# Kernel optimization log

Measured on AMD Instinct MI355X. Metric: run time of the kernel, lower is better.

Reference implementation:

```python
import jax, jax.numpy as jnp
import numpy as np

GROUPS = 8


def setup_inputs() -> dict:
    key = jax.random.key(0)
    k1, k2, k3 = jax.random.split(key, 3)
    B, H, W, Cin, Cout, KH, KW = 32, 56, 56, 256, 256, 3, 3
    inputs = jax.random.normal(k1, (B, H, W, Cin), dtype=jnp.float32)
    # HWIO kernel for grouped conv: input channel dim = Cin // groups
    fan_in = KH * KW * (Cin // GROUPS)
    limit = np.sqrt(6.0 / (fan_in + Cout // GROUPS))  # glorot-ish scale
    kernel = jax.random.uniform(k2, (KH, KW, Cin // GROUPS, Cout), dtype=jnp.float32,
                                minval=-limit, maxval=limit)
    bias = jnp.zeros((Cout,), dtype=jnp.float32)
    return {"inputs": inputs, "kernel": kernel, "bias": bias}


def reference(inputs, kernel, bias):
    # Equivalent to per-group slice + Conv2D + concat: a single grouped conv.
    # inputs: [B,H,W,Cin] NHWC; kernel: [KH,KW,Cin//G,Cout] HWIO
    out = jax.lax.conv_general_dilated(
        inputs, kernel,
        window_strides=(1, 1),
        padding="SAME",
        lhs_dilation=(1, 1),
        rhs_dilation=(1, 1),
        dimension_numbers=("NHWC", "HWIO", "NHWC"),
        feature_group_count=GROUPS,
    )
    out = out + bias  # broadcast over [B,H,W,Cout]
    return out
```

## Files before the change

kernel.cpp:

```cpp
#include <hip/hip_runtime.h>


#define R_ 8
#define TPW 7

typedef __bf16 bf16x8 __attribute__((ext_vector_type(8)));
typedef float floatx4 __attribute__((ext_vector_type(4)));
typedef unsigned short ushortx4 __attribute__((ext_vector_type(4)));

__device__ __forceinline__ unsigned short f2bf(float f) {
    unsigned int u = __builtin_bit_cast(unsigned int, f);
    u += 0x7fffu + ((u >> 16) & 1u);
    return (unsigned short)(u >> 16);
}

__global__ __launch_bounds__(256, 2)
void gconv_mfma(const float* __restrict__ in, const float* __restrict__ wgt,
                const float* __restrict__ bias, float* __restrict__ out) {
    const int rt = blockIdx.x;
    const int g  = blockIdx.y;
    const int b  = blockIdx.z;
    const int y0 = rt * R_;

    __shared__ unsigned short lds_in[10 * 58 * 32];
    __shared__ unsigned short lds_w[9 * 32 * 32];

    const int tid = threadIdx.x;

    for (int i = tid; i < 9 * 32 * 32; i += 256) {
        const int co = i & 31;
        const int ci = (i >> 5) & 31;
        const int kk = i >> 10;
        lds_w[(kk * 32 + co) * 32 + ci] = f2bf(wgt[(kk * 32 + ci) * 256 + g * 32 + co]);
    }

    for (int c = tid; c < 10 * 58 * 8; c += 256) {
        const int row = c / 464;
        const int rem = c - row * 464;
        const int col = rem >> 3;
        const int q   = rem & 7;
        const int gy = y0 - 1 + row;
        const int gx = col - 1;
        float4 v = make_float4(0.f, 0.f, 0.f, 0.f);
        if ((unsigned)gy < 56u && (unsigned)gx < 56u) {
            v = *reinterpret_cast<const float4*>(
                &in[(((b * 56 + gy) * 56 + gx) * 256) + g * 32 + q * 4]);
        }
        ushortx4 p;
        p.x = f2bf(v.x); p.y = f2bf(v.y); p.z = f2bf(v.z); p.w = f2bf(v.w);
        *reinterpret_cast<ushortx4*>(&lds_in[(row * 58 + col) * 32 + q * 4]) = p;
    }

    __syncthreads();

    const int wv   = tid >> 6;
    const int lane = tid & 63;
    const int lc   = lane & 15;
    const int quad = lane >> 4;

    int lane_base[TPW];
#pragma unroll
    for (int t = 0; t < TPW; ++t) {
        const int p  = (wv * TPW + t) * 16 + lc;
        const int yl = p / 56;
        const int xl = p - yl * 56;
        lane_base[t] = (yl * 58 + xl) * 32 + quad * 8;
    }

    floatx4 acc[TPW][2];
#pragma unroll
    for (int t = 0; t < TPW; ++t) {
        acc[t][0] = (floatx4)(0.f);
        acc[t][1] = (floatx4)(0.f);
    }

#pragma unroll
    for (int kk = 0; kk < 9; ++kk) {
        const int ky = kk / 3, kx = kk % 3;
        const int koff = (ky * 58 + kx) * 32;
        const bf16x8 bf0 = *reinterpret_cast<const bf16x8*>(
            &lds_w[(kk * 32 + lc) * 32 + quad * 8]);
        const bf16x8 bf1 = *reinterpret_cast<const bf16x8*>(
            &lds_w[(kk * 32 + 16 + lc) * 32 + quad * 8]);
#pragma unroll
        for (int t = 0; t < TPW; ++t) {
            const bf16x8 a = *reinterpret_cast<const bf16x8*>(&lds_in[lane_base[t] + koff]);
            acc[t][0] = __builtin_amdgcn_mfma_f32_16x16x32_bf16(a, bf0, acc[t][0], 0, 0, 0);
            acc[t][1] = __builtin_amdgcn_mfma_f32_16x16x32_bf16(a, bf1, acc[t][1], 0, 0, 0);
        }
    }

    const float bv0 = bias[g * 32 + lc];
    const float bv1 = bias[g * 32 + 16 + lc];
#pragma unroll
    for (int t = 0; t < TPW; ++t) {
#pragma unroll
        for (int r = 0; r < 4; ++r) {
            const int p = (wv * TPW + t) * 16 + quad * 4 + r;
            const int y = p / 56;
            const int x = p - y * 56;
            float* o = &out[(((b * 56) + y0 + y) * 56 + x) * 256 + g * 32];
            o[lc]      = acc[t][0][r] + bv0;
            o[16 + lc] = acc[t][1][r] + bv1;
        }
    }
}

extern "C" void kernel_launch(void* const* d_in, const int* in_sizes, int n_in,
                              void* d_out, int out_size, void* d_ws, size_t ws_size,
                              hipStream_t stream) {
    const float* in   = (const float*)d_in[0];
    const float* wgt  = (const float*)d_in[1];
    const float* bias = (const float*)d_in[2];
    float* out        = (float*)d_out;
    dim3 grid(7, 8, 32);
    gconv_mfma<<<grid, dim3(256, 1, 1), 0, stream>>>(in, wgt, bias, out);
}
```

Before: 223.2 us.

## Precompute bf16 weights in a prep kernel and stream them from global memory

Measured after the change: 197.6 us. -11.5%, faster.

```diff
diff --git a/kernel.cpp b/kernel.cpp
--- a/kernel.cpp
+++ b/kernel.cpp
@@ -14,8 +14,20 @@
     return (unsigned short)(u >> 16);
 }
 
-__global__ __launch_bounds__(256, 2)
-void gconv_mfma(const float* __restrict__ in, const float* __restrict__ wgt,
+__global__ __launch_bounds__(256)
+void wprep(const float* __restrict__ wgt, unsigned short* __restrict__ wbf) {
+    const int i = blockIdx.x * 256 + threadIdx.x;
+    const int co256 = i & 255;
+    const int tmp   = i >> 8;
+    const int ci    = tmp & 31;
+    const int kk    = tmp >> 5;
+    const int g  = co256 >> 5;
+    const int co = co256 & 31;
+    wbf[((g * 9 + kk) * 32 + co) * 32 + ci] = f2bf(wgt[i]);
+}
+
+__global__ __launch_bounds__(256, 4)
+void gconv_mfma(const float* __restrict__ in, const unsigned short* __restrict__ wbf,
                 const float* __restrict__ bias, float* __restrict__ out) {
     const int rt = blockIdx.x;
     const int g  = blockIdx.y;
@@ -23,16 +35,8 @@
     const int y0 = rt * R_;
 
     __shared__ unsigned short lds_in[10 * 58 * 32];
-    __shared__ unsigned short lds_w[9 * 32 * 32];
 
     const int tid = threadIdx.x;
-
-    for (int i = tid; i < 9 * 32 * 32; i += 256) {
-        const int co = i & 31;
-        const int ci = (i >> 5) & 31;
-        const int kk = i >> 10;
-        lds_w[(kk * 32 + co) * 32 + ci] = f2bf(wgt[(kk * 32 + ci) * 256 + g * 32 + co]);
-    }
 
     for (int c = tid; c < 10 * 58 * 8; c += 256) {
         const int row = c / 464;
@@ -67,6 +71,8 @@
         lane_base[t] = (yl * 58 + xl) * 32 + quad * 8;
     }
 
+    const unsigned short* wq = &wbf[((g * 9) * 32) * 32 + quad * 8];
+
     floatx4 acc[TPW][2];
 #pragma unroll
     for (int t = 0; t < TPW; ++t) {
@@ -74,20 +80,25 @@
         acc[t][1] = (floatx4)(0.f);
     }
 
+    bf16x8 b0 = *reinterpret_cast<const bf16x8*>(&wq[(0 * 32 + lc) * 32]);
+    bf16x8 b1 = *reinterpret_cast<const bf16x8*>(&wq[(0 * 32 + 16 + lc) * 32]);
+
 #pragma unroll
     for (int kk = 0; kk < 9; ++kk) {
         const int ky = kk / 3, kx = kk % 3;
         const int koff = (ky * 58 + kx) * 32;
-        const bf16x8 bf0 = *reinterpret_cast<const bf16x8*>(
-            &lds_w[(kk * 32 + lc) * 32 + quad * 8]);
-        const bf16x8 bf1 = *reinterpret_cast<const bf16x8*>(
-            &lds_w[(kk * 32 + 16 + lc) * 32 + quad * 8]);
+        bf16x8 nb0 = b0, nb1 = b1;
+        if (kk < 8) {
+            nb0 = *reinterpret_cast<const bf16x8*>(&wq[((kk + 1) * 32 + lc) * 32]);
+            nb1 = *reinterpret_cast<const bf16x8*>(&wq[((kk + 1) * 32 + 16 + lc) * 32]);
+        }
 #pragma unroll
         for (int t = 0; t < TPW; ++t) {
             const bf16x8 a = *reinterpret_cast<const bf16x8*>(&lds_in[lane_base[t] + koff]);
-            acc[t][0] = __builtin_amdgcn_mfma_f32_16x16x32_bf16(a, bf0, acc[t][0], 0, 0, 0);
-            acc[t][1] = __builtin_amdgcn_mfma_f32_16x16x32_bf16(a, bf1, acc[t][1], 0, 0, 0);
+            acc[t][0] = __builtin_amdgcn_mfma_f32_16x16x32_bf16(a, b0, acc[t][0], 0, 0, 0);
+            acc[t][1] = __builtin_amdgcn_mfma_f32_16x16x32_bf16(a, b1, acc[t][1], 0, 0, 0);
         }
+        b0 = nb0; b1 = nb1;
     }
 
     const float bv0 = bias[g * 32 + lc];
@@ -106,6 +117,66 @@
     }
 }
 
+__global__ __launch_bounds__(256, 2)
+void gconv_mfma_ldsw(const float* __restrict__ in, const float* __restrict__ wgt,
+                     const float* __restrict__ bias, float* __restrict__ out) {
+    const int rt = blockIdx.x, g = blockIdx.y, b = blockIdx.z;
+    const int y0 = rt * R_;
+    __shared__ unsigned short lds_in[10 * 58 * 32];
+    __shared__ unsigned short lds_w[9 * 32 * 32];
+    const int tid = threadIdx.x;
+    for (int i = tid; i < 9 * 32 * 32; i += 256) {
+        const int co = i & 31, ci = (i >> 5) & 31, kk = i >> 10;
+        lds_w[(kk * 32 + co) * 32 + ci] = f2bf(wgt[(kk * 32 + ci) * 256 + g * 32 + co]);
+    }
+    for (int c = tid; c < 10 * 58 * 8; c += 256) {
+        const int row = c / 464, rem = c - row * 464, col = rem >> 3, q = rem & 7;
+        const int gy = y0 - 1 + row, gx = col - 1;
+        float4 v = make_float4(0.f, 0.f, 0.f, 0.f);
+        if ((unsigned)gy < 56u && (unsigned)gx < 56u)
+            v = *reinterpret_cast<const float4*>(&in[(((b * 56 + gy) * 56 + gx) * 256) + g * 32 + q * 4]);
+        ushortx4 p;
+        p.x = f2bf(v.x); p.y = f2bf(v.y); p.z = f2bf(v.z); p.w = f2bf(v.w);
+        *reinterpret_cast<ushortx4*>(&lds_in[(row * 58 + col) * 32 + q * 4]) = p;
+    }
+    __syncthreads();
+    const int wv = tid >> 6, lane = tid & 63, lc = lane & 15, quad = lane >> 4;
+    int lane_base[TPW];
+#pragma unroll
+    for (int t = 0; t < TPW; ++t) {
+        const int p = (wv * TPW + t) * 16 + lc;
+        const int yl = p / 56, xl = p - yl * 56;
+        lane_base[t] = (yl * 58 + xl) * 32 + quad * 8;
+    }
+    floatx4 acc[TPW][2];
+#pragma unroll
+    for (int t = 0; t < TPW; ++t) { acc[t][0] = (floatx4)(0.f); acc[t][1] = (floatx4)(0.f); }
+#pragma unroll
+    for (int kk = 0; kk < 9; ++kk) {
+        const int ky = kk / 3, kx = kk % 3;
+        const int koff = (ky * 58 + kx) * 32;
+        const bf16x8 bf0 = *reinterpret_cast<const bf16x8*>(&lds_w[(kk * 32 + lc) * 32 + quad * 8]);
+        const bf16x8 bf1 = *reinterpret_cast<const bf16x8*>(&lds_w[(kk * 32 + 16 + lc) * 32 + quad * 8]);
+#pragma unroll
+        for (int t = 0; t < TPW; ++t) {
+            const bf16x8 a = *reinterpret_cast<const bf16x8*>(&lds_in[lane_base[t] + koff]);
+            acc[t][0] = __builtin_amdgcn_mfma_f32_16x16x32_bf16(a, bf0, acc[t][0], 0, 0, 0);
+            acc[t][1] = __builtin_amdgcn_mfma_f32_16x16x32_bf16(a, bf1, acc[t][1], 0, 0, 0);
+        }
+    }
+    const float bv0 = bias[g * 32 + lc], bv1 = bias[g * 32 + 16 + lc];
+#pragma unroll
+    for (int t = 0; t < TPW; ++t)
+#pragma unroll
+        for (int r = 0; r < 4; ++r) {
+            const int p = (wv * TPW + t) * 16 + quad * 4 + r;
+            const int y = p / 56, x = p - y * 56;
+            float* o = &out[(((b * 56) + y0 + y) * 56 + x) * 256 + g * 32];
+            o[lc] = acc[t][0][r] + bv0;
+            o[16 + lc] = acc[t][1][r] + bv1;
+        }
+}
+
 extern "C" void kernel_launch(void* const* d_in, const int* in_sizes, int n_in,
                               void* d_out, int out_size, void* d_ws, size_t ws_size,
                               hipStream_t stream) {
@@ -114,5 +185,12 @@
     const float* bias = (const float*)d_in[2];
     float* out        = (float*)d_out;
     dim3 grid(7, 8, 32);
-    gconv_mfma<<<grid, dim3(256, 1, 1), 0, stream>>>(in, wgt, bias, out);
+
+    if (ws_size >= (size_t)(8 * 9 * 32 * 32 * sizeof(unsigned short))) {
+        unsigned short* wbf = (unsigned short*)d_ws;
+        wprep<<<dim3(288, 1, 1), dim3(256, 1, 1), 0, stream>>>(wgt, wbf);
+        gconv_mfma<<<grid, dim3(256, 1, 1), 0, stream>>>(in, wbf, bias, out);
+    } else {
+        gconv_mfma_ldsw<<<grid, dim3(256, 1, 1), 0, stream>>>(in, wgt, bias, out);
+    }
 }
```
